# Kernel tuning notes

Measured on AMD Instinct MI355X. Metric: run time of the kernel, lower is better.

The kernel has to match this reference:

```python
import jax, jax.numpy as jnp
from jax import lax
import numpy as np

B, T, IN, H, NC, NL = 128, 256, 64, 256, 1, 2


def _lstm_dir(x, w_ih, w_hh, b_ih, b_hh, reverse):
    """Single-direction LSTM over x:[B,T,in]. PyTorch gate order i,f,g,o."""
    Bd = x.shape[0]
    Hd = w_hh.shape[1]
    # precompute input contribution to gates: [T,B,4H]
    xg = jnp.einsum('bti,gi->tbg', x, w_ih) + b_ih + b_hh

    def step(carry, xg_t):
        h, c = carry
        g = xg_t + h @ w_hh.T                      # [B,4H]
        i, f, gg, o = jnp.split(g, 4, axis=-1)
        i = jax.nn.sigmoid(i)
        f = jax.nn.sigmoid(f)
        gg = jnp.tanh(gg)
        o = jax.nn.sigmoid(o)
        c = f * c + i * gg
        h = o * jnp.tanh(c)
        return (h, c), h

    h0 = jnp.zeros((Bd, Hd), x.dtype)
    _, hs = lax.scan(step, (h0, h0), xg, reverse=reverse)
    return jnp.swapaxes(hs, 0, 1)                  # [B,T,H], time-aligned


def _bilstm(x, params):
    out = x
    for l in range(NL):
        fwd = _lstm_dir(out, params[f'w_ih_l{l}f'], params[f'w_hh_l{l}f'],
                        params[f'b_ih_l{l}f'], params[f'b_hh_l{l}f'], reverse=False)
        bwd = _lstm_dir(out, params[f'w_ih_l{l}b'], params[f'w_hh_l{l}b'],
                        params[f'b_ih_l{l}b'], params[f'b_hh_l{l}b'], reverse=True)
        out = jnp.concatenate([fwd, bwd], axis=-1)  # [B,T,2H]
        # (nn.LSTM dropout=0.2 is train-only between layers; eval -> identity)
    return out


def setup_inputs() -> dict:
    key = jax.random.key(0)
    ks = iter(jax.random.split(key, 32))
    inp = {'x': jax.random.normal(next(ks), (B, T, IN), jnp.float32)}
    s = 1.0 / np.sqrt(H)
    for l in range(NL):
        isz = IN if l == 0 else 2 * H
        for d in ('f', 'b'):
            inp[f'w_ih_l{l}{d}'] = jax.random.uniform(next(ks), (4 * H, isz), jnp.float32, -s, s)
            inp[f'w_hh_l{l}{d}'] = jax.random.uniform(next(ks), (4 * H, H), jnp.float32, -s, s)
            inp[f'b_ih_l{l}{d}'] = jax.random.uniform(next(ks), (4 * H,), jnp.float32, -s, s)
            inp[f'b_hh_l{l}{d}'] = jax.random.uniform(next(ks), (4 * H,), jnp.float32, -s, s)
    inp['fc_w'] = jax.random.uniform(next(ks), (NC, 2 * H), jnp.float32, -s, s)
    inp['fc_b'] = jax.random.uniform(next(ks), (NC,), jnp.float32, -s, s)
    return inp


def reference(x,
              w_ih_l0f, w_hh_l0f, b_ih_l0f, b_hh_l0f,
              w_ih_l0b, w_hh_l0b, b_ih_l0b, b_hh_l0b,
              w_ih_l1f, w_hh_l1f, b_ih_l1f, b_hh_l1f,
              w_ih_l1b, w_hh_l1b, b_ih_l1b, b_hh_l1b,
              fc_w, fc_b):
    params = dict(w_ih_l0f=w_ih_l0f, w_hh_l0f=w_hh_l0f, b_ih_l0f=b_ih_l0f, b_hh_l0f=b_hh_l0f,
                  w_ih_l0b=w_ih_l0b, w_hh_l0b=w_hh_l0b, b_ih_l0b=b_ih_l0b, b_hh_l0b=b_hh_l0b,
                  w_ih_l1f=w_ih_l1f, w_hh_l1f=w_hh_l1f, b_ih_l1f=b_ih_l1f, b_hh_l1f=b_hh_l1f,
                  w_ih_l1b=w_ih_l1b, w_hh_l1b=w_hh_l1b, b_ih_l1b=b_ih_l1b, b_hh_l1b=b_hh_l1b)
    out = _bilstm(x, params)          # [B,T,2H]
    last = out[:, -1, :]              # [B,2H]
    return last @ fc_w.T + fc_b       # [B,NC]
```

## Files before the change

### kernel.cpp

```cpp
#include <hip/hip_runtime.h>


typedef unsigned long long ull;

constexpr int B_ = 128, T_ = 256, IN_ = 64, H_ = 256;
constexpr int JW = 64;

#define KEEP_REG(x) asm volatile("" : "+v"(x))

__device__ __forceinline__ float sigmoid_(float x) { return 1.f / (1.f + __expf(-x)); }
__device__ __forceinline__ float tanh_(float x)    { return 1.f - 2.f / (1.f + __expf(2.f * x)); }
__device__ __forceinline__ int hidx(int k) { return (k >> 6) * 68 + (k & 63); }
__device__ __forceinline__ int widx(int gp, int jl, int ks, int kp) {
  return ((gp * 64 + jl) * 4 + ks) * 68 + kp;
}

template<int BB, bool L0M>
__global__ __launch_bounds__(256, 1)
void recur(const float* __restrict__ whh_f, const float* __restrict__ whh_b,
           const float* __restrict__ wih_f, const float* __restrict__ wih_b,
           const float* __restrict__ bih_f, const float* __restrict__ bhh_f,
           const float* __restrict__ bih_b, const float* __restrict__ bhh_b,
           const float* __restrict__ x,
           const float* __restrict__ xg,
           float* __restrict__ out0,
           float* __restrict__ hstate, float* __restrict__ cstate,
           float* __restrict__ hfinal,
           ull* __restrict__ ring,
           int ngroup, int dir_base, int nsteps, int step_base,
           int first, int save, int lastW)
{
  const int bid = blockIdx.x;
  const int kw  = bid & 3;
  const int gr  = (bid >> 2) % ngroup;
  const int dl  = (bid >> 2) / ngroup;
  const int d   = dir_base + dl;
  const int tid = threadIdx.x;
  const int jl  = tid >> 2;
  const int ks  = tid & 3;
  const int j   = kw * JW + jl;
  const int bbase = gr * BB;
  const int gidx  = dl * ngroup + gr;

  const float* whh  = d ? whh_b : whh_f;
  const float* wihp = d ? wih_b : wih_f;

  float wr[2][64];
  #pragma unroll
  for (int g = 0; g < 2; ++g) {
    const float* wrow = whh + (long)(g * H_ + j) * H_ + ks * 64;
    #pragma unroll
    for (int q = 0; q < 16; ++q) {
      const float4 w4 = *(const float4*)(wrow + q * 4);
      wr[g][q*4+0] = w4.x; wr[g][q*4+1] = w4.y;
      wr[g][q*4+2] = w4.z; wr[g][q*4+3] = w4.w;
    }
  }
  #pragma unroll
  for (int g = 0; g < 2; ++g)
    #pragma unroll
    for (int q = 0; q < 64; ++q) KEEP_REG(wr[g][q]);

  __shared__ alignas(16) float wlds[2 * 64 * 4 * 68];
  __shared__ alignas(16) float hbuf[2][BB][272];
  __shared__ alignas(16) float xt[2][4][64];
  #pragma unroll
  for (int gp = 0; gp < 2; ++gp) {
    const float* wrow = whh + (long)((gp + 2) * H_ + j) * H_ + ks * 64;
    float* dst = &wlds[widx(gp, jl, ks, 0)];
    #pragma unroll
    for (int q = 0; q < 16; ++q)
      *(float4*)(dst + q * 4) = *(const float4*)(wrow + q * 4);
  }

  float br[4];
  if constexpr (L0M) {
    const float* bih = d ? bih_b : bih_f;
    const float* bhh = d ? bhh_b : bhh_f;
    #pragma unroll
    for (int g = 0; g < 4; ++g) br[g] = bih[g * H_ + j] + bhh[g * H_ + j];
  }

  for (int idx = tid; idx < BB * H_; idx += 256) {
    const int b = idx >> 8, k = idx & 255;
    hbuf[0][b][hidx(k)] = first ? 0.f : hstate[(long)(bbase + b) * H_ + k];
  }
  float cs[BB];
  #pragma unroll
  for (int b = 0; b < BB; ++b)
    cs[b] = first ? 0.f : cstate[(long)(bbase + b) * H_ + j];

  if constexpr (L0M) {
    if (tid < BB * 64) {
      const int b = tid >> 6, kx = tid & 63;
      const int t0 = d ? T_ - 1 : 0;
      xt[0][b][kx] = x[((long)(bbase + b) * T_ + t0) * IN_ + kx];
    }
  }
  float xr[BB][4], xn[BB][4];
  if constexpr (!L0M) {
    #pragma unroll
    for (int b = 0; b < BB; ++b)
      #pragma unroll
      for (int g = 0; g < 4; ++g)
        xr[b][g] = xg[(long)(bbase + b) * 1024 + g * H_ + j];
  }
  __syncthreads();

  const long ringstride = (long)2 * BB * H_;
  constexpr int NP = 3 * JW * BB;
  constexpr int NL = (NP + 255) / 256;

  for (int s = 0; s < nsteps; ++s) {
    const int p = s & 1, wp = p ^ 1;
    const int gstep = step_base + s;

    float4 wa_[2][4], wb_[2][4];
    if constexpr (L0M) {
      #pragma unroll
      for (int gp = 0; gp < 2; ++gp) {
        const float* wa = wihp + (long)((2 * gp) * H_ + j) * IN_ + ks * 16;
        const float* wb = wihp + (long)((2 * gp + 1) * H_ + j) * IN_ + ks * 16;
        #pragma unroll
        for (int q = 0; q < 4; ++q) {
          wa_[gp][q] = *(const float4*)(wa + q * 4);
          wb_[gp][q] = *(const float4*)(wb + q * 4);
        }
      }
    }

    float xpre = 0.f;
    if constexpr (L0M) {
      if (s + 1 < nsteps && tid < BB * 64) {
        const int b = tid >> 6, kx = tid & 63;
        const int ttn = d ? (T_ - 2 - s) : (s + 1);
        xpre = x[((long)(bbase + b) * T_ + ttn) * IN_ + kx];
      }
    } else {
      const int sn = (s + 1 < nsteps) ? s + 1 : s;
      #pragma unroll
      for (int b = 0; b < BB; ++b)
        #pragma unroll
        for (int g = 0; g < 4; ++g)
          xn[b][g] = xg[((long)sn * B_ + bbase + b) * 1024 + g * H_ + j];
    }

    ull vv[NL];
    if (s > 0) {
      const long roff = gidx * ringstride + (long)((gstep - 1) & 1) * (BB * H_);
      #pragma unroll
      for (int q = 0; q < NL; ++q) {
        const int pidx = tid + q * 256;
        if (pidx < NP) {
          const int psl = pidx / (JW * BB), rem = pidx % (JW * BB);
          const int kwp = psl + (psl >= kw ? 1 : 0);
          vv[q] = __hip_atomic_load(ring + roff + (rem >> 6) * H_
                                        + kwp * JW + (rem & 63),
                                    __ATOMIC_RELAXED, __HIP_MEMORY_SCOPE_AGENT);
        }
      }
    }

    float acc[BB][4];
    #pragma unroll
    for (int b = 0; b < BB; ++b)
      #pragma unroll
      for (int g = 0; g < 4; ++g) acc[b][g] = 0.f;

    if constexpr (L0M) {
      #pragma unroll
      for (int gp = 0; gp < 2; ++gp) {
        const int g0 = 2 * gp, g1 = 2 * gp + 1;
        #pragma unroll
        for (int b = 0; b < BB; ++b) {
          #pragma unroll
          for (int q = 0; q < 4; ++q) {
            const float4 xv = *(const float4*)&xt[p][b][ks * 16 + q * 4];
            acc[b][g0] = fmaf(xv.x, wa_[gp][q].x, acc[b][g0]);
            acc[b][g0] = fmaf(xv.y, wa_[gp][q].y, acc[b][g0]);
            acc[b][g0] = fmaf(xv.z, wa_[gp][q].z, acc[b][g0]);
            acc[b][g0] = fmaf(xv.w, wa_[gp][q].w, acc[b][g0]);
            acc[b][g1] = fmaf(xv.x, wb_[gp][q].x, acc[b][g1]);
            acc[b][g1] = fmaf(xv.y, wb_[gp][q].y, acc[b][g1]);
            acc[b][g1] = fmaf(xv.z, wb_[gp][q].z, acc[b][g1]);
            acc[b][g1] = fmaf(xv.w, wb_[gp][q].w, acc[b][g1]);
          }
        }
      }
      if (s + 1 < nsteps && tid < BB * 64) {
        const int b = tid >> 6, kx = tid & 63;
        xt[wp][b][kx] = xpre;
      }
    }

    if (s > 0) {
      const unsigned want = (unsigned)gstep;
      const long roff = gidx * ringstride + (long)((gstep - 1) & 1) * (BB * H_);
      long gd = 0;
      for (;;) {
        bool ok = true;
        #pragma unroll
        for (int q = 0; q < NL; ++q)
          if (tid + q * 256 < NP && (unsigned)(vv[q] >> 32) != want) ok = false;
        if (ok) break;
        if (++gd > (1L << 20)) break;
        __builtin_amdgcn_s_sleep(1);
        #pragma unroll
        for (int q = 0; q < NL; ++q) {
          const int pidx = tid + q * 256;
          if (pidx < NP && (unsigned)(vv[q] >> 32) != want) {
            const int psl = pidx / (JW * BB), rem = pidx % (JW * BB);
            const int kwp = psl + (psl >= kw ? 1 : 0);
            vv[q] = __hip_atomic_load(ring + roff + (rem >> 6) * H_
                                          + kwp * JW + (rem & 63),
                                      __ATOMIC_RELAXED, __HIP_MEMORY_SCOPE_AGENT);
          }
        }
      }
      #pragma unroll
      for (int q = 0; q < NL; ++q) {
        const int pidx = tid + q * 256;
        if (pidx < NP) {
          const int psl = pidx / (JW * BB), rem = pidx % (JW * BB);
          const int kwp = psl + (psl >= kw ? 1 : 0);
          hbuf[p][rem >> 6][hidx(kwp * JW + (rem & 63))] =
              __uint_as_float((unsigned)vv[q]);
        }
      }
    }
    __syncthreads();

    #pragma unroll
    for (int q = 0; q < 16; ++q) {
      const float4 wg = *(const float4*)&wlds[widx(0, jl, ks, q * 4)];
      const float4 wo = *(const float4*)&wlds[widx(1, jl, ks, q * 4)];
      #pragma unroll
      for (int b = 0; b < BB; ++b) {
        const float4 hv = *(const float4*)&hbuf[p][b][ks * 68 + q * 4];
        acc[b][0] = fmaf(hv.x, wr[0][q*4+0], acc[b][0]);
        acc[b][0] = fmaf(hv.y, wr[0][q*4+1], acc[b][0]);
        acc[b][0] = fmaf(hv.z, wr[0][q*4+2], acc[b][0]);
        acc[b][0] = fmaf(hv.w, wr[0][q*4+3], acc[b][0]);
        acc[b][1] = fmaf(hv.x, wr[1][q*4+0], acc[b][1]);
        acc[b][1] = fmaf(hv.y, wr[1][q*4+1], acc[b][1]);
        acc[b][1] = fmaf(hv.z, wr[1][q*4+2], acc[b][1]);
        acc[b][1] = fmaf(hv.w, wr[1][q*4+3], acc[b][1]);
        acc[b][2] = fmaf(hv.x, wg.x, acc[b][2]);
        acc[b][2] = fmaf(hv.y, wg.y, acc[b][2]);
        acc[b][2] = fmaf(hv.z, wg.z, acc[b][2]);
        acc[b][2] = fmaf(hv.w, wg.w, acc[b][2]);
        acc[b][3] = fmaf(hv.x, wo.x, acc[b][3]);
        acc[b][3] = fmaf(hv.y, wo.y, acc[b][3]);
        acc[b][3] = fmaf(hv.z, wo.z, acc[b][3]);
        acc[b][3] = fmaf(hv.w, wo.w, acc[b][3]);
      }
    }

    float hv_[BB];
    #pragma unroll
    for (int b = 0; b < BB; ++b) {
      #pragma unroll
      for (int g = 0; g < 4; ++g) {
        float a = acc[b][g];
        a += __shfl_xor(a, 1, 64);
        a += __shfl_xor(a, 2, 64);
        if constexpr (L0M) acc[b][g] = a + br[g];
        else               acc[b][g] = a + xr[b][g];
      }
      const float ig = sigmoid_(acc[b][0]);
      const float fg = sigmoid_(acc[b][1]);
      const float gg = tanh_(acc[b][2]);
      const float og = sigmoid_(acc[b][3]);
      cs[b] = fg * cs[b] + ig * gg;
      hv_[b] = og * tanh_(cs[b]);
    }

    if (ks < BB) {
      float hmine = hv_[0], cmine = cs[0];
      #pragma unroll
      for (int b = 1; b < BB; ++b)
        if (ks == b) { hmine = hv_[b]; cmine = cs[b]; }

      if (s < nsteps - 1) {
        const ull pv = ((ull)(unsigned)(gstep + 1) << 32)
                     | (unsigned)__float_as_uint(hmine);
        __hip_atomic_store(ring + gidx * ringstride
                               + (long)(gstep & 1) * (BB * H_) + ks * H_ + j,
                           pv, __ATOMIC_RELAXED, __HIP_MEMORY_SCOPE_AGENT);
      }
      hbuf[wp][ks][hidx(j)] = hmine;

      if constexpr (L0M) {
        const int tt = d ? (T_ - 1 - gstep) : gstep;
        out0[((long)tt * B_ + bbase + ks) * 512 + d * H_ + j] = hmine;
      } else {
        if (s == nsteps - 1 && lastW)
          hfinal[(long)(bbase + ks) * 512 + (d ? H_ : 0) + j] = hmine;
      }
      if (save && s == nsteps - 1) {
        hstate[(long)(bbase + ks) * H_ + j] = hmine;
        cstate[(long)(bbase + ks) * H_ + j] = cmine;
      }
    }

    if constexpr (!L0M) {
      #pragma unroll
      for (int b = 0; b < BB; ++b)
        #pragma unroll
        for (int g = 0; g < 4; ++g) xr[b][g] = xn[b][g];
    }
  }
}

__global__ __launch_bounds__(256, 2)
void xg_gemm(const float* __restrict__ A, const float* __restrict__ W,
             const float* __restrict__ b1, const float* __restrict__ b2,
             float* __restrict__ C)
{
  __shared__ float As[16][128];
  __shared__ float Bs[16][132];
  const int tid = threadIdx.x;
  const int tx = tid & 15, ty = tid >> 4;
  const long m0 = (long)blockIdx.x * 128;
  const int  n0 = blockIdx.y * 128;
  const int sr = tid >> 1;
  const int sk = (tid & 1) * 8;
  const float* Ar = A + (m0 + sr) * 512 + sk;
  const float* Wr = W + (long)(n0 + sr) * 512 + sk;
  float acc[8][8];
  #pragma unroll
  for (int i = 0; i < 8; ++i)
    #pragma unroll
    for (int jj = 0; jj < 8; ++jj) acc[i][jj] = 0.f;

  for (int k0 = 0; k0 < 512; k0 += 16) {
    const float4 a0 = *(const float4*)(Ar + k0);
    const float4 a1 = *(const float4*)(Ar + k0 + 4);
    const float4 w0 = *(const float4*)(Wr + k0);
    const float4 w1 = *(const float4*)(Wr + k0 + 4);
    __syncthreads();
    As[sk+0][sr]=a0.x; As[sk+1][sr]=a0.y; As[sk+2][sr]=a0.z; As[sk+3][sr]=a0.w;
    As[sk+4][sr]=a1.x; As[sk+5][sr]=a1.y; As[sk+6][sr]=a1.z; As[sk+7][sr]=a1.w;
    Bs[sk+0][sr]=w0.x; Bs[sk+1][sr]=w0.y; Bs[sk+2][sr]=w0.z; Bs[sk+3][sr]=w0.w;
    Bs[sk+4][sr]=w1.x; Bs[sk+5][sr]=w1.y; Bs[sk+6][sr]=w1.z; Bs[sk+7][sr]=w1.w;
    __syncthreads();
    #pragma unroll
    for (int k = 0; k < 16; ++k) {
      const float4 av0 = *(const float4*)&As[k][ty * 8];
      const float4 av1 = *(const float4*)&As[k][ty * 8 + 4];
      const float4 bv0 = *(const float4*)&Bs[k][tx * 8];
      const float4 bv1 = *(const float4*)&Bs[k][tx * 8 + 4];
      const float a_[8] = {av0.x,av0.y,av0.z,av0.w,av1.x,av1.y,av1.z,av1.w};
      const float b_[8] = {bv0.x,bv0.y,bv0.z,bv0.w,bv1.x,bv1.y,bv1.z,bv1.w};
      #pragma unroll
      for (int i = 0; i < 8; ++i)
        #pragma unroll
        for (int jj = 0; jj < 8; ++jj)
          acc[i][jj] = fmaf(a_[i], b_[jj], acc[i][jj]);
    }
  }
  float bsum[8];
  #pragma unroll
  for (int jj = 0; jj < 8; ++jj) {
    const int col = n0 + tx * 8 + jj;
    bsum[jj] = b1[col] + b2[col];
  }
  #pragma unroll
  for (int i = 0; i < 8; ++i) {
    const long crow = m0 + ty * 8 + i;
    #pragma unroll
    for (int q = 0; q < 2; ++q) {
      float4 o;
      o.x = acc[i][q*4+0] + bsum[q*4+0];
      o.y = acc[i][q*4+1] + bsum[q*4+1];
      o.z = acc[i][q*4+2] + bsum[q*4+2];
      o.w = acc[i][q*4+3] + bsum[q*4+3];
      *(float4*)&C[crow * 1024 + n0 + tx * 8 + q * 4] = o;
    }
  }
}

__global__ void fc_kernel(const float* __restrict__ hfinal,
                          const float* __restrict__ fc_w,
                          const float* __restrict__ fc_b,
                          float* __restrict__ out)
{
  const int tid = threadIdx.x;
  const int b = tid >> 2, q = tid & 3;
  float s = 0.f;
  const float* hp = hfinal + b * 512 + q * 128;
  const float* wp = fc_w + q * 128;
  #pragma unroll 4
  for (int k = 0; k < 128; ++k) s += hp[k] * wp[k];
  s += __shfl_xor(s, 1, 64);
  s += __shfl_xor(s, 2, 64);
  if (q == 0) out[b] = s + fc_b[0];
}

extern "C" void kernel_launch(void* const* d_in, const int* in_sizes, int n_in,
                              void* d_out, int out_size, void* d_ws, size_t ws_size,
                              hipStream_t stream)
{
  const float* x     = (const float*)d_in[0];
  const float* wih0f = (const float*)d_in[1];
  const float* whh0f = (const float*)d_in[2];
  const float* bih0f = (const float*)d_in[3];
  const float* bhh0f = (const float*)d_in[4];
  const float* wih0b = (const float*)d_in[5];
  const float* whh0b = (const float*)d_in[6];
  const float* bih0b = (const float*)d_in[7];
  const float* bhh0b = (const float*)d_in[8];
  const float* wih1f = (const float*)d_in[9];
  const float* whh1f = (const float*)d_in[10];
  const float* bih1f = (const float*)d_in[11];
  const float* bhh1f = (const float*)d_in[12];
  const float* wih1b = (const float*)d_in[13];
  const float* whh1b = (const float*)d_in[14];
  const float* bih1b = (const float*)d_in[15];
  const float* bhh1b = (const float*)d_in[16];
  const float* fcw   = (const float*)d_in[17];
  const float* fcb   = (const float*)d_in[18];

  const size_t n_out0 = (size_t)T_ * B_ * 512;
  const size_t nring0 = 64ull * 2 * 4 * 256;
  const size_t nring1 = 64ull * 2 * 2 * 256;
  const size_t ringB  = (nring0 + nring1) * sizeof(ull);
  const size_t fixedf = n_out0 + (size_t)B_ * 1024 + 2 * (size_t)B_ * 256
                      + (size_t)B_ * 512;

  int CH = 0; bool full = false;
  if (4 * (fixedf + (size_t)T_ * B_ * 1024) + ringB <= ws_size) {
    full = true; CH = T_;
  } else {
    const int cands[4] = {64, 32, 16, 8};
    for (int i = 0; i < 4; ++i)
      if (4 * (fixedf + (size_t)cands[i] * B_ * 1024) + ringB <= ws_size) {
        CH = cands[i]; break;
      }
  }
  if (!CH) return;

  float* out0 = (float*)d_ws;
  float* xga  = out0 + n_out0;
  float* xg1b = xga + (size_t)CH * B_ * 1024;
  float* hst1 = xg1b + (size_t)B_ * 1024;
  float* cst1 = hst1 + (size_t)B_ * 256;
  float* hfin = cst1 + (size_t)B_ * 256;
  ull*  ring0 = (ull*)(hfin + (size_t)B_ * 512);
  ull*  ring1 = ring0 + nring0;

  hipMemsetAsync(ring0, 0, ringB, stream);

  recur<4, true><<<dim3(256), dim3(256), 0, stream>>>(
      whh0f, whh0b, wih0f, wih0b, bih0f, bhh0f, bih0b, bhh0b,
      x, nullptr, out0, nullptr, nullptr, nullptr, ring0,
      32, 0, T_, 0,
      1, 0, 0);

  xg_gemm<<<dim3(1, 8), dim3(256), 0, stream>>>(
      out0 + (size_t)(T_ - 1) * B_ * 512, wih1b, bih1b, bhh1b, xg1b);
  recur<2, false><<<dim3(256), dim3(256), 0, stream>>>(
      whh1f, whh1b, nullptr, nullptr, nullptr, nullptr, nullptr, nullptr,
      nullptr, xg1b, nullptr, hst1, cst1, hfin, ring1,
      64, 1, 1, 0,
      1, 0, 1);

  if (full) {
    xg_gemm<<<dim3(T_ * B_ / 128, 8), dim3(256), 0, stream>>>(
        out0, wih1f, bih1f, bhh1f, xga);
    recur<2, false><<<dim3(256), dim3(256), 0, stream>>>(
        whh1f, whh1b, nullptr, nullptr, nullptr, nullptr, nullptr, nullptr,
        nullptr, xga, nullptr, hst1, cst1, hfin, ring1,
        64, 0, T_, 0,
        1, 0, 1);
  } else {
    const int nch = T_ / CH;
    for (int c = 0; c < nch; ++c) {
      xg_gemm<<<dim3(CH * B_ / 128, 8), dim3(256), 0, stream>>>(
          out0 + (size_t)c * CH * B_ * 512, wih1f, bih1f, bhh1f, xga);
      recur<2, false><<<dim3(256), dim3(256), 0, stream>>>(
          whh1f, whh1b, nullptr, nullptr, nullptr, nullptr, nullptr, nullptr,
          nullptr, xga, nullptr, hst1, cst1, hfin, ring1,
          64, 0, CH, c * CH,
          c == 0 ? 1 : 0, 1, c == nch - 1 ? 1 : 0);
    }
  }

  fc_kernel<<<dim3(1), dim3(512), 0, stream>>>(hfin, fcw, fcb, (float*)d_out);
}
```

Measured before the change: 2.566 ms.

## Compute layer-1 forward input projection with split-bf16 MFMA GEMM

Replaces the FP32 SIMT GEMM for the layer-1 forward input-gate projection with an MFMA kernel. Both operands are first split into high and low bf16 planes, and three bf16 MFMAs per tile are summed to keep close to FP32 accuracy. It adds a conversion pass over the weights and over each activation chunk, plus workspace for the bf16 planes. The MFMA kernel loads operands straight from global memory without LDS staging, so its memory efficiency is uncertain.

Result: slower. 2.753 ms (+7.3%).

```diff
diff --git a/kernel.cpp b/kernel.cpp
--- a/kernel.cpp
+++ b/kernel.cpp
@@ -2,6 +2,8 @@
 
 
 typedef unsigned long long ull;
+typedef __attribute__((ext_vector_type(8))) short bf16x8;
+typedef __attribute__((ext_vector_type(4))) float f32x4;
 
 constexpr int B_ = 128, T_ = 256, IN_ = 64, H_ = 256;
 constexpr int JW = 64;
@@ -380,6 +382,70 @@
   }
 }
 
+__global__ __launch_bounds__(256)
+void cvt_planes(const float* __restrict__ src,
+                unsigned* __restrict__ hp, unsigned* __restrict__ lp, long n2)
+{
+  long i = (long)blockIdx.x * 256 + threadIdx.x;
+  const long stride = (long)gridDim.x * 256;
+  for (; i < n2; i += stride) {
+    const float a0 = src[2 * i], a1 = src[2 * i + 1];
+    const unsigned u0 = __float_as_uint(a0), u1 = __float_as_uint(a1);
+    const unsigned h0 = (u0 + 0x7fffu + ((u0 >> 16) & 1u)) >> 16;
+    const unsigned h1 = (u1 + 0x7fffu + ((u1 >> 16) & 1u)) >> 16;
+    const float d0 = a0 - __uint_as_float(h0 << 16);
+    const float d1 = a1 - __uint_as_float(h1 << 16);
+    const unsigned ud0 = __float_as_uint(d0), ud1 = __float_as_uint(d1);
+    const unsigned l0 = (ud0 + 0x7fffu + ((ud0 >> 16) & 1u)) >> 16;
+    const unsigned l1 = (ud1 + 0x7fffu + ((ud1 >> 16) & 1u)) >> 16;
+    hp[i] = h0 | (h1 << 16);
+    lp[i] = l0 | (l1 << 16);
+  }
+}
+
+__global__ __launch_bounds__(256, 2)
+void xg_mfma(const unsigned short* __restrict__ Ah, const unsigned short* __restrict__ Al,
+             const unsigned short* __restrict__ Wh, const unsigned short* __restrict__ Wl,
+             const float* __restrict__ b1, const float* __restrict__ b2,
+             float* __restrict__ C)
+{
+  const int tid = threadIdx.x;
+  const int w = tid >> 6, l = tid & 63;
+  const int lr = l & 15, lg = l >> 4;
+  const long m0 = (long)blockIdx.x * 64 + w * 16;
+  const int  n0 = blockIdx.y * 128;
+
+  f32x4 acc[8];
+  #pragma unroll
+  for (int nt = 0; nt < 8; ++nt) acc[nt] = (f32x4){0.f, 0.f, 0.f, 0.f};
+
+  const long abase = (m0 + lr) * 512 + lg * 8;
+  for (int k0 = 0; k0 < 512; k0 += 32) {
+    const bf16x8 a_h = *(const bf16x8*)(Ah + abase + k0);
+    const bf16x8 a_l = *(const bf16x8*)(Al + abase + k0);
+    #pragma unroll
+    for (int nt = 0; nt < 8; ++nt) {
+      const long wbase = (long)(n0 + nt * 16 + lr) * 512 + lg * 8 + k0;
+      const bf16x8 b_h = *(const bf16x8*)(Wh + wbase);
+      const bf16x8 b_l = *(const bf16x8*)(Wl + wbase);
+      acc[nt] = __builtin_amdgcn_mfma_f32_16x16x32_bf16(a_h, b_h, acc[nt], 0, 0, 0);
+      acc[nt] = __builtin_amdgcn_mfma_f32_16x16x32_bf16(a_h, b_l, acc[nt], 0, 0, 0);
+      acc[nt] = __builtin_amdgcn_mfma_f32_16x16x32_bf16(a_l, b_h, acc[nt], 0, 0, 0);
+    }
+  }
+
+  #pragma unroll
+  for (int nt = 0; nt < 8; ++nt) {
+    const int col = n0 + nt * 16 + lr;
+    const float bs = b1[col] + b2[col];
+    #pragma unroll
+    for (int r = 0; r < 4; ++r) {
+      const long row = m0 + lg * 4 + r;
+      C[row * 1024 + col] = acc[nt][r] + bs;
+    }
+  }
+}
+
 __global__ void fc_kernel(const float* __restrict__ hfinal,
                           const float* __restrict__ fc_w,
                           const float* __restrict__ fc_b,
@@ -427,27 +493,30 @@
   const size_t ringB  = (nring0 + nring1) * sizeof(ull);
   const size_t fixedf = n_out0 + (size_t)B_ * 1024 + 2 * (size_t)B_ * 256
                       + (size_t)B_ * 512;
-
-  int CH = 0; bool full = false;
-  if (4 * (fixedf + (size_t)T_ * B_ * 1024) + ringB <= ws_size) {
-    full = true; CH = T_;
-  } else {
-    const int cands[4] = {64, 32, 16, 8};
-    for (int i = 0; i < 4; ++i)
-      if (4 * (fixedf + (size_t)cands[i] * B_ * 1024) + ringB <= ws_size) {
-        CH = cands[i]; break;
-      }
-  }
+  const size_t wplaneB = 2ull * 1024 * 512 * 2;
+
+  auto needB = [&](size_t ch) {
+    const size_t aplaneB = 2ull * ch * B_ * 512 * 2;
+    return 4 * (fixedf + ch * B_ * 1024) + ringB + wplaneB + aplaneB + 256;
+  };
+  size_t CH = 0;
+  const size_t cands[5] = {(size_t)T_, 64, 32, 16, 8};
+  for (int i = 0; i < 5; ++i)
+    if (needB(cands[i]) <= ws_size) { CH = cands[i]; break; }
   if (!CH) return;
 
   float* out0 = (float*)d_ws;
   float* xga  = out0 + n_out0;
-  float* xg1b = xga + (size_t)CH * B_ * 1024;
+  float* xg1b = xga + CH * B_ * 1024;
   float* hst1 = xg1b + (size_t)B_ * 1024;
   float* cst1 = hst1 + (size_t)B_ * 256;
   float* hfin = cst1 + (size_t)B_ * 256;
   ull*  ring0 = (ull*)(hfin + (size_t)B_ * 512);
   ull*  ring1 = ring0 + nring0;
+  unsigned short* Whp = (unsigned short*)(ring1 + nring1);
+  unsigned short* Wlp = Whp + (size_t)1024 * 512;
+  unsigned short* Ahp = Wlp + (size_t)1024 * 512;
+  unsigned short* Alp = Ahp + CH * B_ * 512;
 
   hipMemsetAsync(ring0, 0, ringB, stream);
 
@@ -456,6 +525,9 @@
       x, nullptr, out0, nullptr, nullptr, nullptr, ring0,
       32, 0, T_, 0,
       1, 0, 0);
+
+  cvt_planes<<<dim3(256), dim3(256), 0, stream>>>(
+      wih1f, (unsigned*)Whp, (unsigned*)Wlp, (long)1024 * 512 / 2);
 
   xg_gemm<<<dim3(1, 8), dim3(256), 0, stream>>>(
       out0 + (size_t)(T_ - 1) * B_ * 512, wih1b, bih1b, bhh1b, xg1b);
@@ -465,25 +537,18 @@
       64, 1, 1, 0,
       1, 0, 1);
 
-  if (full) {
-    xg_gemm<<<dim3(T_ * B_ / 128, 8), dim3(256), 0, stream>>>(
-        out0, wih1f, bih1f, bhh1f, xga);
+  const int nch = (int)(T_ / CH);
+  for (int c = 0; c < nch; ++c) {
+    cvt_planes<<<dim3(2048), dim3(256), 0, stream>>>(
+        out0 + (size_t)c * CH * B_ * 512,
+        (unsigned*)Ahp, (unsigned*)Alp, (long)CH * B_ * 512 / 2);
+    xg_mfma<<<dim3((unsigned)(CH * B_ / 64), 8), dim3(256), 0, stream>>>(
+        Ahp, Alp, Whp, Wlp, bih1f, bhh1f, xga);
     recur<2, false><<<dim3(256), dim3(256), 0, stream>>>(
         whh1f, whh1b, nullptr, nullptr, nullptr, nullptr, nullptr, nullptr,
         nullptr, xga, nullptr, hst1, cst1, hfin, ring1,
-        64, 0, T_, 0,
-        1, 0, 1);
-  } else {
-    const int nch = T_ / CH;
-    for (int c = 0; c < nch; ++c) {
-      xg_gemm<<<dim3(CH * B_ / 128, 8), dim3(256), 0, stream>>>(
-          out0 + (size_t)c * CH * B_ * 512, wih1f, bih1f, bhh1f, xga);
-      recur<2, false><<<dim3(256), dim3(256), 0, stream>>>(
-          whh1f, whh1b, nullptr, nullptr, nullptr, nullptr, nullptr, nullptr,
-          nullptr, xga, nullptr, hst1, cst1, hfin, ring1,
-          64, 0, CH, c * CH,
-          c == 0 ? 1 : 0, 1, c == nch - 1 ? 1 : 0);
-    }
+        64, 0, (int)CH, (int)(c * CH),
+        c == 0 ? 1 : 0, 1, c == nch - 1 ? 1 : 0);
   }
 
   fc_kernel<<<dim3(1), dim3(512), 0, stream>>>(hfin, fcw, fcb, (float*)d_out);
```

## Split recurrent K-reduction across 8 lanes with 512-thread blocks

Applied to the files above, without the earlier changes.

Doubles the threads per recurrent block from 256 to 512, so each hidden unit's dot product over H is split eight ways instead of four. Each thread now holds half as many W_hh registers and LDS slices, and the reduction gains one more shuffle stage. The layer-0 input projection is restructured to load W_ih per gate inside the step rather than hoisting all of it. The aim is more latency hiding and less per-thread serial FMA work on the latency-bound recurrence. The cost is an extra cross-lane shuffle per gate and more threads taking part in each barrier and ring-polling step.

Measured after the change: 2.319 ms. 1.11x faster.

```diff
diff --git a/kernel.cpp b/kernel.cpp
--- a/kernel.cpp
+++ b/kernel.cpp
@@ -10,13 +10,13 @@
 
 __device__ __forceinline__ float sigmoid_(float x) { return 1.f / (1.f + __expf(-x)); }
 __device__ __forceinline__ float tanh_(float x)    { return 1.f - 2.f / (1.f + __expf(2.f * x)); }
-__device__ __forceinline__ int hidx(int k) { return (k >> 6) * 68 + (k & 63); }
+__device__ __forceinline__ int hidx(int k) { return (k >> 5) * 36 + (k & 31); }
 __device__ __forceinline__ int widx(int gp, int jl, int ks, int kp) {
-  return ((gp * 64 + jl) * 4 + ks) * 68 + kp;
+  return ((gp * 64 + jl) * 8 + ks) * 36 + kp;
 }
 
 template<int BB, bool L0M>
-__global__ __launch_bounds__(256, 1)
+__global__ __launch_bounds__(512, 1)
 void recur(const float* __restrict__ whh_f, const float* __restrict__ whh_b,
            const float* __restrict__ wih_f, const float* __restrict__ wih_b,
            const float* __restrict__ bih_f, const float* __restrict__ bhh_f,
@@ -36,8 +36,8 @@
   const int dl  = (bid >> 2) / ngroup;
   const int d   = dir_base + dl;
   const int tid = threadIdx.x;
-  const int jl  = tid >> 2;
-  const int ks  = tid & 3;
+  const int jl  = tid >> 3;
+  const int ks  = tid & 7;
   const int j   = kw * JW + jl;
   const int bbase = gr * BB;
   const int gidx  = dl * ngroup + gr;
@@ -45,12 +45,12 @@
   const float* whh  = d ? whh_b : whh_f;
   const float* wihp = d ? wih_b : wih_f;
 
-  float wr[2][64];
+  float wr[2][32];
   #pragma unroll
   for (int g = 0; g < 2; ++g) {
-    const float* wrow = whh + (long)(g * H_ + j) * H_ + ks * 64;
-    #pragma unroll
-    for (int q = 0; q < 16; ++q) {
+    const float* wrow = whh + (long)(g * H_ + j) * H_ + ks * 32;
+    #pragma unroll
+    for (int q = 0; q < 8; ++q) {
       const float4 w4 = *(const float4*)(wrow + q * 4);
       wr[g][q*4+0] = w4.x; wr[g][q*4+1] = w4.y;
       wr[g][q*4+2] = w4.z; wr[g][q*4+3] = w4.w;
@@ -59,17 +59,17 @@
   #pragma unroll
   for (int g = 0; g < 2; ++g)
     #pragma unroll
-    for (int q = 0; q < 64; ++q) KEEP_REG(wr[g][q]);
-
-  __shared__ alignas(16) float wlds[2 * 64 * 4 * 68];
-  __shared__ alignas(16) float hbuf[2][BB][272];
+    for (int q = 0; q < 32; ++q) KEEP_REG(wr[g][q]);
+
+  __shared__ alignas(16) float wlds[2 * 64 * 8 * 36];
+  __shared__ alignas(16) float hbuf[2][BB][288];
   __shared__ alignas(16) float xt[2][4][64];
   #pragma unroll
   for (int gp = 0; gp < 2; ++gp) {
-    const float* wrow = whh + (long)((gp + 2) * H_ + j) * H_ + ks * 64;
+    const float* wrow = whh + (long)((gp + 2) * H_ + j) * H_ + ks * 32;
     float* dst = &wlds[widx(gp, jl, ks, 0)];
     #pragma unroll
-    for (int q = 0; q < 16; ++q)
+    for (int q = 0; q < 8; ++q)
       *(float4*)(dst + q * 4) = *(const float4*)(wrow + q * 4);
   }
 
@@ -81,7 +81,7 @@
     for (int g = 0; g < 4; ++g) br[g] = bih[g * H_ + j] + bhh[g * H_ + j];
   }
 
-  for (int idx = tid; idx < BB * H_; idx += 256) {
+  for (int idx = tid; idx < BB * H_; idx += 512) {
     const int b = idx >> 8, k = idx & 255;
     hbuf[0][b][hidx(k)] = first ? 0.f : hstate[(long)(bbase + b) * H_ + k];
   }
@@ -109,25 +109,11 @@
 
   const long ringstride = (long)2 * BB * H_;
   constexpr int NP = 3 * JW * BB;
-  constexpr int NL = (NP + 255) / 256;
+  constexpr int NL = (NP + 511) / 512;
 
   for (int s = 0; s < nsteps; ++s) {
     const int p = s & 1, wp = p ^ 1;
     const int gstep = step_base + s;
-
-    float4 wa_[2][4], wb_[2][4];
-    if constexpr (L0M) {
-      #pragma unroll
-      for (int gp = 0; gp < 2; ++gp) {
-        const float* wa = wihp + (long)((2 * gp) * H_ + j) * IN_ + ks * 16;
-        const float* wb = wihp + (long)((2 * gp + 1) * H_ + j) * IN_ + ks * 16;
-        #pragma unroll
-        for (int q = 0; q < 4; ++q) {
-          wa_[gp][q] = *(const float4*)(wa + q * 4);
-          wb_[gp][q] = *(const float4*)(wb + q * 4);
-        }
-      }
-    }
 
     float xpre = 0.f;
     if constexpr (L0M) {
@@ -150,7 +136,7 @@
       const long roff = gidx * ringstride + (long)((gstep - 1) & 1) * (BB * H_);
       #pragma unroll
       for (int q = 0; q < NL; ++q) {
-        const int pidx = tid + q * 256;
+        const int pidx = tid + q * 512;
         if (pidx < NP) {
           const int psl = pidx / (JW * BB), rem = pidx % (JW * BB);
           const int kwp = psl + (psl >= kw ? 1 : 0);
@@ -169,22 +155,22 @@
 
     if constexpr (L0M) {
       #pragma unroll
-      for (int gp = 0; gp < 2; ++gp) {
-        const int g0 = 2 * gp, g1 = 2 * gp + 1;
+      for (int g = 0; g < 4; ++g) {
+        const float* wa = wihp + (long)(g * H_ + j) * IN_ + ks * 8;
+        const float4 w0 = *(const float4*)(wa);
+        const float4 w1 = *(const float4*)(wa + 4);
         #pragma unroll
         for (int b = 0; b < BB; ++b) {
-          #pragma unroll
-          for (int q = 0; q < 4; ++q) {
-            const float4 xv = *(const float4*)&xt[p][b][ks * 16 + q * 4];
-            acc[b][g0] = fmaf(xv.x, wa_[gp][q].x, acc[b][g0]);
-            acc[b][g0] = fmaf(xv.y, wa_[gp][q].y, acc[b][g0]);
-            acc[b][g0] = fmaf(xv.z, wa_[gp][q].z, acc[b][g0]);
-            acc[b][g0] = fmaf(xv.w, wa_[gp][q].w, acc[b][g0]);
-            acc[b][g1] = fmaf(xv.x, wb_[gp][q].x, acc[b][g1]);
-            acc[b][g1] = fmaf(xv.y, wb_[gp][q].y, acc[b][g1]);
-            acc[b][g1] = fmaf(xv.z, wb_[gp][q].z, acc[b][g1]);
-            acc[b][g1] = fmaf(xv.w, wb_[gp][q].w, acc[b][g1]);
-          }
+          const float4 x0 = *(const float4*)&xt[p][b][ks * 8];
+          const float4 x1 = *(const float4*)&xt[p][b][ks * 8 + 4];
+          acc[b][g] = fmaf(x0.x, w0.x, acc[b][g]);
+          acc[b][g] = fmaf(x0.y, w0.y, acc[b][g]);
+          acc[b][g] = fmaf(x0.z, w0.z, acc[b][g]);
+          acc[b][g] = fmaf(x0.w, w0.w, acc[b][g]);
+          acc[b][g] = fmaf(x1.x, w1.x, acc[b][g]);
+          acc[b][g] = fmaf(x1.y, w1.y, acc[b][g]);
+          acc[b][g] = fmaf(x1.z, w1.z, acc[b][g]);
+          acc[b][g] = fmaf(x1.w, w1.w, acc[b][g]);
         }
       }
       if (s + 1 < nsteps && tid < BB * 64) {
@@ -201,13 +187,13 @@
         bool ok = true;
         #pragma unroll
         for (int q = 0; q < NL; ++q)
-          if (tid + q * 256 < NP && (unsigned)(vv[q] >> 32) != want) ok = false;
+          if (tid + q * 512 < NP && (unsigned)(vv[q] >> 32) != want) ok = false;
         if (ok) break;
         if (++gd > (1L << 20)) break;
         __builtin_amdgcn_s_sleep(1);
         #pragma unroll
         for (int q = 0; q < NL; ++q) {
-          const int pidx = tid + q * 256;
+          const int pidx = tid + q * 512;
           if (pidx < NP && (unsigned)(vv[q] >> 32) != want) {
             const int psl = pidx / (JW * BB), rem = pidx % (JW * BB);
             const int kwp = psl + (psl >= kw ? 1 : 0);
@@ -219,7 +205,7 @@
       }
       #pragma unroll
       for (int q = 0; q < NL; ++q) {
-        const int pidx = tid + q * 256;
+        const int pidx = tid + q * 512;
         if (pidx < NP) {
           const int psl = pidx / (JW * BB), rem = pidx % (JW * BB);
           const int kwp = psl + (psl >= kw ? 1 : 0);
@@ -231,12 +217,12 @@
     __syncthreads();
 
     #pragma unroll
-    for (int q = 0; q < 16; ++q) {
+    for (int q = 0; q < 8; ++q) {
       const float4 wg = *(const float4*)&wlds[widx(0, jl, ks, q * 4)];
       const float4 wo = *(const float4*)&wlds[widx(1, jl, ks, q * 4)];
       #pragma unroll
       for (int b = 0; b < BB; ++b) {
-        const float4 hv = *(const float4*)&hbuf[p][b][ks * 68 + q * 4];
+        const float4 hv = *(const float4*)&hbuf[p][b][ks * 36 + q * 4];
         acc[b][0] = fmaf(hv.x, wr[0][q*4+0], acc[b][0]);
         acc[b][0] = fmaf(hv.y, wr[0][q*4+1], acc[b][0]);
         acc[b][0] = fmaf(hv.z, wr[0][q*4+2], acc[b][0]);
@@ -264,6 +250,7 @@
         float a = acc[b][g];
         a += __shfl_xor(a, 1, 64);
         a += __shfl_xor(a, 2, 64);
+        a += __shfl_xor(a, 4, 64);
         if constexpr (L0M) acc[b][g] = a + br[g];
         else               acc[b][g] = a + xr[b][g];
       }
@@ -451,7 +438,7 @@
 
   hipMemsetAsync(ring0, 0, ringB, stream);
 
-  recur<4, true><<<dim3(256), dim3(256), 0, stream>>>(
+  recur<4, true><<<dim3(256), dim3(512), 0, stream>>>(
       whh0f, whh0b, wih0f, wih0b, bih0f, bhh0f, bih0b, bhh0b,
       x, nullptr, out0, nullptr, nullptr, nullptr, ring0,
       32, 0, T_, 0,
@@ -459,7 +446,7 @@
 
   xg_gemm<<<dim3(1, 8), dim3(256), 0, stream>>>(
       out0 + (size_t)(T_ - 1) * B_ * 512, wih1b, bih1b, bhh1b, xg1b);
-  recur<2, false><<<dim3(256), dim3(256), 0, stream>>>(
+  recur<2, false><<<dim3(256), dim3(512), 0, stream>>>(
       whh1f, whh1b, nullptr, nullptr, nullptr, nullptr, nullptr, nullptr,
       nullptr, xg1b, nullptr, hst1, cst1, hfin, ring1,
       64, 1, 1, 0,
@@ -468,7 +455,7 @@
   if (full) {
     xg_gemm<<<dim3(T_ * B_ / 128, 8), dim3(256), 0, stream>>>(
         out0, wih1f, bih1f, bhh1f, xga);
-    recur<2, false><<<dim3(256), dim3(256), 0, stream>>>(
+    recur<2, false><<<dim3(256), dim3(512), 0, stream>>>(
         whh1f, whh1b, nullptr, nullptr, nullptr, nullptr, nullptr, nullptr,
         nullptr, xga, nullptr, hst1, cst1, hfin, ring1,
         64, 0, T_, 0,
@@ -478,7 +465,7 @@
     for (int c = 0; c < nch; ++c) {
       xg_gemm<<<dim3(CH * B_ / 128, 8), dim3(256), 0, stream>>>(
           out0 + (size_t)c * CH * B_ * 512, wih1f, bih1f, bhh1f, xga);
-      recur<2, false><<<dim3(256), dim3(256), 0, stream>>>(
+      recur<2, false><<<dim3(256), dim3(512), 0, stream>>>(
           whh1f, whh1b, nullptr, nullptr, nullptr, nullptr, nullptr, nullptr,
           nullptr, xga, nullptr, hst1, cst1, hfin, ring1,
           64, 0, CH, c * CH,
```
